# Optimization experiments

Measured on AMD Instinct MI355X. Metric: run time of the kernel, lower is better.

The kernel has to match this reference:

```python
import jax, jax.numpy as jnp
import numpy as np

THRESHOLD = 0.1
EPS = 1e-05


def setup_inputs() -> dict:
    key = jax.random.key(0)
    kx, kl, k1, k2 = jax.random.split(key, 4)
    B, S, D = 8, 4096, 1024
    Dh = max(2, D // 2)
    x = jax.random.normal(kx, (B, S, D), dtype=jnp.float32)
    # trailing (right) padding with random valid lengths in [S//2, S]
    lengths = jax.random.randint(kl, (B,), S // 2, S + 1)
    pad = jnp.arange(S)[None, :] >= lengths[:, None]  # [B, S] bool, True = padded
    W1 = jax.random.normal(k1, (D, Dh), dtype=jnp.float32) * (1.0 / np.sqrt(D))
    b1 = jnp.zeros((Dh,), dtype=jnp.float32)
    W2 = jax.random.normal(k2, (Dh, 1), dtype=jnp.float32) * (1.0 / np.sqrt(Dh))
    b2 = jnp.zeros((1,), dtype=jnp.float32)
    return {"x": x, "pad": pad, "W1": W1, "b1": b1, "W2": W2, "b2": b2}


def reference(x, pad, W1, b1, W2, b2):
    B, S, D = x.shape
    pos = jnp.arange(S)
    # number of valid (non-pad) tokens per batch; pad is trailing
    length = S - jnp.sum(pad, axis=1)  # [B]

    # tiny gate MLP: Linear -> ReLU -> Linear, squashed to (0, 1)
    h = jax.nn.relu(jnp.einsum('bsd,dh->bsh', x, W1) + b1)
    y = jnp.einsum('bsh,ho->bso', h, W2) + b2          # [B, S, 1]
    y = (1.0 + jnp.tanh(10.0 * y)) * 0.5

    # zero out gate values at padded positions (torch loop: y[i, n:] = 0)
    valid = pos[None, :] < length[:, None]             # [B, S]
    y = jnp.where(valid[..., None], y, 0.0)

    # lift so at least one token passes the threshold
    adjust = jnp.clip(EPS + THRESHOLD - jnp.max(y, axis=1), 0.0)  # [B, 1]
    y = y + adjust[:, None, :]                         # broadcast over seq

    u = x * y                                          # gated features [B, S, D]
    ys = y[..., 0]                                     # [B, S]
    u_mask = (ys > THRESHOLD) & (~pad)                 # tokens kept
    new_len = jnp.sum(u_mask, axis=1)                  # [B]

    # compact kept tokens to the front of each row (stable sort: kept first,
    # original order preserved) -- the mask-scatter v[v_mask] = u[u_mask]
    order = jnp.argsort(~u_mask, axis=1, stable=True)  # [B, S]
    v = jnp.take_along_axis(u, order[..., None], axis=1)
    v_mask = pos[None, :] < new_len[:, None]           # [B, S]
    v = jnp.where(v_mask[..., None], v, 0.0)
    v_pad = ~v_mask
    return v, v_pad
```

## Files before the change

kernel.cpp:

```cpp
#include <hip/hip_runtime.h>
#include <math.h>

#define NB 8
#define NS 4096
#define ND 1024
#define NDH 512
#define NTOK (NB*NS)
#define THRESH 0.1f
#define EPSV 1e-5f

using short8   = __attribute__((ext_vector_type(8)))  short;
using floatx16 = __attribute__((ext_vector_type(16))) float;

__device__ __forceinline__ unsigned short f32_to_bf16_rne(float f) {
  union { float f; unsigned u; } v; v.f = f;
  unsigned r = v.u + 0x7fffu + ((v.u >> 16) & 1u);
  return (unsigned short)(r >> 16);
}
__device__ __forceinline__ float bf16_to_f32(unsigned short h) {
  union { unsigned u; float f; } v; v.u = ((unsigned)h) << 16;
  return v.f;
}

__global__ __launch_bounds__(256)
void k0_prep(const float* __restrict__ W1, unsigned short* __restrict__ Wf,
             unsigned int* __restrict__ rowmax) {
  __shared__ float sw[16][513];
  const int t = threadIdx.x;
  const int k16 = blockIdx.x;
  if (k16 == 0 && t < NB) rowmax[t] = 0u;
#pragma unroll
  for (int i = 0; i < 8; ++i) {
    int flat = i * 256 + t;
    int r = flat >> 7, c4 = (flat & 127) << 2;
    *(float4*)&sw[r][c4] = *(const float4*)(W1 + (size_t)(k16 * 16 + r) * NDH + c4);
  }
  __syncthreads();
#pragma unroll
  for (int q = 0; q < 4; ++q) {
    int ss = q * 256 + t;
    int n32 = ss >> 6, lane = ss & 63;
    int n = n32 * 32 + (lane & 31);
    int kb = (lane >> 5) * 8;
    unsigned hi2[4], lo2[4];
#pragma unroll
    for (int j = 0; j < 4; ++j) {
      float w0 = sw[kb + 2 * j][n], w1 = sw[kb + 2 * j + 1][n];
      unsigned short h0 = f32_to_bf16_rne(w0), h1 = f32_to_bf16_rne(w1);
      unsigned short l0 = f32_to_bf16_rne(w0 - bf16_to_f32(h0));
      unsigned short l1 = f32_to_bf16_rne(w1 - bf16_to_f32(h1));
      hi2[j] = (unsigned)h0 | ((unsigned)h1 << 16);
      lo2[j] = (unsigned)l0 | ((unsigned)l1 << 16);
    }
    size_t cb = ((size_t)(n32 * 64 + k16) * 2) * 512 + (size_t)lane * 8;
    *(uint4*)(Wf + cb)       = make_uint4(hi2[0], hi2[1], hi2[2], hi2[3]);
    *(uint4*)(Wf + cb + 512) = make_uint4(lo2[0], lo2[1], lo2[2], lo2[3]);
  }
}

__global__ __launch_bounds__(256, 2)
void k1_gemm(const float* __restrict__ x, const unsigned short* __restrict__ Wf,
             const float* __restrict__ b1, const float* __restrict__ W2,
             float* __restrict__ ylin) {
  __shared__ __align__(16) unsigned short sx[2][2][64 * 40];
  __shared__ float red[4][64];

  const int tid = threadIdx.x;
  const int wave = tid >> 6, lane = tid & 63;
  const int l31 = lane & 31, h5 = lane >> 5;
  const int tok0 = blockIdx.x * 64;

  floatx16 acc[2][4];
#pragma unroll
  for (int mt = 0; mt < 2; ++mt)
#pragma unroll
    for (int nt = 0; nt < 4; ++nt)
#pragma unroll
      for (int r = 0; r < 16; ++r) acc[mt][nt][r] = 0.f;

  const int sm = tid >> 2;
  const int sk = (tid & 3) * 8;
  const float* xrow = x + (size_t)(tok0 + sm) * ND + sk;

  const unsigned short* wb[4];
#pragma unroll
  for (int nt = 0; nt < 4; ++nt)
    wb[nt] = Wf + (((size_t)(wave * 4 + nt) * 64) * 2) * 512 + (size_t)lane * 8;

  for (int it = 0; it < 32; ++it) {
    const int p = it & 1;
    short8 bh[4][2], bl[4][2];
#pragma unroll
    for (int nt = 0; nt < 4; ++nt)
#pragma unroll
      for (int kh = 0; kh < 2; ++kh) {
        const unsigned short* q = wb[nt] + ((size_t)(2 * it + kh) * 2) * 512;
        bh[nt][kh] = *(const short8*)(q);
        bl[nt][kh] = *(const short8*)(q + 512);
      }
    {
      const float* xp = xrow + it * 32;
      float4 xa = *(const float4*)xp;
      float4 xb = *(const float4*)(xp + 4);
      float v8[8] = {xa.x, xa.y, xa.z, xa.w, xb.x, xb.y, xb.z, xb.w};
      unsigned hp[4], lp[4];
#pragma unroll
      for (int j = 0; j < 4; ++j) {
        unsigned short h0 = f32_to_bf16_rne(v8[2 * j]);
        unsigned short h1 = f32_to_bf16_rne(v8[2 * j + 1]);
        unsigned short l0 = f32_to_bf16_rne(v8[2 * j] - bf16_to_f32(h0));
        unsigned short l1 = f32_to_bf16_rne(v8[2 * j + 1] - bf16_to_f32(h1));
        hp[j] = (unsigned)h0 | ((unsigned)h1 << 16);
        lp[j] = (unsigned)l0 | ((unsigned)l1 << 16);
      }
      *(uint4*)&sx[p][0][sm * 40 + sk] = make_uint4(hp[0], hp[1], hp[2], hp[3]);
      *(uint4*)&sx[p][1][sm * 40 + sk] = make_uint4(lp[0], lp[1], lp[2], lp[3]);
    }
    __syncthreads();
    short8 ah[2][2], al[2][2];
#pragma unroll
    for (int mt = 0; mt < 2; ++mt)
#pragma unroll
      for (int kh = 0; kh < 2; ++kh) {
        ah[mt][kh] = *(const short8*)&sx[p][0][(mt * 32 + l31) * 40 + kh * 16 + h5 * 8];
        al[mt][kh] = *(const short8*)&sx[p][1][(mt * 32 + l31) * 40 + kh * 16 + h5 * 8];
      }
#pragma unroll
    for (int kh = 0; kh < 2; ++kh)
#pragma unroll
      for (int nt = 0; nt < 4; ++nt)
#pragma unroll
        for (int mt = 0; mt < 2; ++mt) {
          acc[mt][nt] = __builtin_amdgcn_mfma_f32_32x32x16_bf16(ah[mt][kh], bh[nt][kh], acc[mt][nt], 0, 0, 0);
          acc[mt][nt] = __builtin_amdgcn_mfma_f32_32x32x16_bf16(al[mt][kh], bh[nt][kh], acc[mt][nt], 0, 0, 0);
          acc[mt][nt] = __builtin_amdgcn_mfma_f32_32x32x16_bf16(ah[mt][kh], bl[nt][kh], acc[mt][nt], 0, 0, 0);
        }
  }

  float b1v[4], w2v[4];
#pragma unroll
  for (int nt = 0; nt < 4; ++nt) {
    const int n = wave * 128 + nt * 32 + l31;
    b1v[nt] = b1[n];
    w2v[nt] = W2[n];
  }
#pragma unroll
  for (int mt = 0; mt < 2; ++mt) {
    float pr[16];
#pragma unroll
    for (int r = 0; r < 16; ++r) pr[r] = 0.f;
#pragma unroll
    for (int nt = 0; nt < 4; ++nt)
#pragma unroll
      for (int r = 0; r < 16; ++r)
        pr[r] += fmaxf(acc[mt][nt][r] + b1v[nt], 0.f) * w2v[nt];
#pragma unroll
    for (int m = 1; m <= 16; m <<= 1)
#pragma unroll
      for (int r = 0; r < 16; ++r) pr[r] += __shfl_xor(pr[r], m, 64);
    if (l31 == 0) {
#pragma unroll
      for (int r = 0; r < 16; ++r) {
        int row = (r & 3) + 8 * (r >> 2) + 4 * h5;
        red[wave][mt * 32 + row] = pr[r];
      }
    }
  }
  __syncthreads();
  if (tid < 64)
    ylin[tok0 + tid] = red[0][tid] + red[1][tid] + red[2][tid] + red[3][tid];
}

__global__ __launch_bounds__(256)
void k2a(const float* __restrict__ ylin, const int* __restrict__ pad,
         const float* __restrict__ b2, float* __restrict__ ysq,
         unsigned int* __restrict__ rowmax) {
  __shared__ float wm[4];
  const int t = blockIdx.x * 256 + threadIdx.x;
  float yl = ylin[t] + b2[0];
  float y = (1.f + tanhf(10.f * yl)) * 0.5f;
  if (pad[t]) y = 0.f;
  ysq[t] = y;
  float m = y;
#pragma unroll
  for (int s = 32; s >= 1; s >>= 1) m = fmaxf(m, __shfl_xor(m, s, 64));
  if ((threadIdx.x & 63) == 0) wm[threadIdx.x >> 6] = m;
  __syncthreads();
  if (threadIdx.x == 0) {
    float bm = fmaxf(fmaxf(wm[0], wm[1]), fmaxf(wm[2], wm[3]));
    atomicMax(rowmax + (t >> 12), __float_as_uint(bm));
  }
}

__global__ __launch_bounds__(256)
void k2b(const float* __restrict__ ysq, const int* __restrict__ pad,
         const unsigned int* __restrict__ rowmax, float* __restrict__ yfin,
         int* __restrict__ src_of_dest, int* __restrict__ new_len,
         float* __restrict__ vpad_out) {
  __shared__ int scnt[256];
  const int b = blockIdx.x, tid = threadIdx.x;
  const int base = b * NS, s0 = tid * 16;
  const float adj = fmaxf(EPSV + THRESH - __uint_as_float(rowmax[b]), 0.f);

  float yv[16];
  unsigned km = 0;
  int cnt = 0;
#pragma unroll
  for (int i = 0; i < 16; ++i) {
    int s = s0 + i;
    float yf = ysq[base + s] + adj;
    yv[i] = yf;
    bool keep = (yf > THRESH) && !pad[base + s];
    if (keep) { km |= (1u << i); ++cnt; }
  }
  scnt[tid] = cnt;
  __syncthreads();
  for (int o = 1; o < 256; o <<= 1) {
    int add = (tid >= o) ? scnt[tid - o] : 0;
    __syncthreads();
    scnt[tid] += add;
    __syncthreads();
  }
  const int total = scnt[255];
  int off = scnt[tid] - cnt;
#pragma unroll
  for (int i = 0; i < 16; ++i) {
    int s = s0 + i;
    yfin[base + s] = yv[i];
    if ((km >> i) & 1u) { src_of_dest[base + off] = s; ++off; }
    vpad_out[base + s] = (s >= total) ? 1.f : 0.f;
  }
  if (tid == 0) new_len[b] = total;
}

__global__ __launch_bounds__(256)
void k3_gather(const float* __restrict__ x, const float* __restrict__ yfin,
               const int* __restrict__ src_of_dest, const int* __restrict__ new_len,
               float* __restrict__ v) {
  const int slot0 = blockIdx.x * 4;
  const int b = slot0 >> 12;
  const int nl = new_len[b];
  const int tid = threadIdx.x;
#pragma unroll
  for (int i = 0; i < 4; ++i) {
    const int slot = slot0 + i;
    const int dest = slot & (NS - 1);
    float4* vo = (float4*)(v + (size_t)slot * ND);
    if (dest < nl) {
      const int src = src_of_dest[slot];
      const float g = yfin[b * NS + src];
      const float4* xi = (const float4*)(x + ((size_t)b * NS + src) * ND);
      float4 xv = xi[tid];
      vo[tid] = make_float4(xv.x * g, xv.y * g, xv.z * g, xv.w * g);
    } else {
      vo[tid] = make_float4(0.f, 0.f, 0.f, 0.f);
    }
  }
}

extern "C" void kernel_launch(void* const* d_in, const int* in_sizes, int n_in,
                              void* d_out, int out_size, void* d_ws, size_t ws_size,
                              hipStream_t stream) {
  const float* x   = (const float*)d_in[0];
  const int*   pad = (const int*)d_in[1];
  const float* W1  = (const float*)d_in[2];
  const float* b1  = (const float*)d_in[3];
  const float* W2  = (const float*)d_in[4];
  const float* b2  = (const float*)d_in[5];

  float* v    = (float*)d_out;
  float* vpad = v + (size_t)NTOK * ND;

  unsigned short* Wf = (unsigned short*)(v + 24000000);
  float* ysq = v + 26000000;

  float* ylin = (float*)d_ws;
  float* yfin = ylin + NTOK;
  int* src    = (int*)(yfin + NTOK);
  int* nlen   = src + NTOK;
  unsigned int* rowmax = (unsigned int*)(nlen + NB);

  k0_prep<<<64, 256, 0, stream>>>(W1, Wf, rowmax);
  k1_gemm<<<NTOK / 64, 256, 0, stream>>>(x, Wf, b1, W2, ylin);
  k2a<<<NTOK / 256, 256, 0, stream>>>(ylin, pad, b2, ysq, rowmax);
  k2b<<<NB, 256, 0, stream>>>(ysq, pad, rowmax, yfin, src, nlen, vpad);
  k3_gather<<<NTOK / 4, 256, 0, stream>>>(x, yfin, src, nlen, v);
}
```

Before: 321.9 us.

## Prefetch next x tile in GEMM, fuse gate epilogue, streamline scan and gather

The GEMM loop now prefetches the next K-slice of x into registers and converts it into the other shared buffer while MFMAs run, leaving a single barrier per iteration. The separate tanh/mask/rowmax kernel is folded into the GEMM epilogue, which drops one launch and the ylin round trip. The prefix scan in k2b uses wave shuffles instead of a barrier-heavy shared-memory scan and writes gate values compacted by destination. The gather processes 16 slots per block with nontemporal stores. Risks are more register pressure in the GEMM and more atomics on rowmax, one per 64-token block.

Result: no change. 323.5 us (+0.5%).

```diff
diff --git a/kernel.cpp b/kernel.cpp
--- a/kernel.cpp
+++ b/kernel.cpp
@@ -11,6 +11,7 @@
 
 using short8   = __attribute__((ext_vector_type(8)))  short;
 using floatx16 = __attribute__((ext_vector_type(16))) float;
+using floatv4  = __attribute__((ext_vector_type(4)))  float;
 
 __device__ __forceinline__ unsigned short f32_to_bf16_rne(float f) {
   union { float f; unsigned u; } v; v.f = f;
@@ -61,7 +62,8 @@
 __global__ __launch_bounds__(256, 2)
 void k1_gemm(const float* __restrict__ x, const unsigned short* __restrict__ Wf,
              const float* __restrict__ b1, const float* __restrict__ W2,
-             float* __restrict__ ylin) {
+             const int* __restrict__ pad, const float* __restrict__ b2,
+             float* __restrict__ ysq, unsigned int* __restrict__ rowmax) {
   __shared__ __align__(16) unsigned short sx[2][2][64 * 40];
   __shared__ float red[4][64];
 
@@ -87,8 +89,27 @@
   for (int nt = 0; nt < 4; ++nt)
     wb[nt] = Wf + (((size_t)(wave * 4 + nt) * 64) * 2) * 512 + (size_t)lane * 8;
 
+  {
+    float4 xa = *(const float4*)xrow;
+    float4 xb = *(const float4*)(xrow + 4);
+    float v8[8] = {xa.x, xa.y, xa.z, xa.w, xb.x, xb.y, xb.z, xb.w};
+    unsigned hp[4], lp[4];
+#pragma unroll
+    for (int j = 0; j < 4; ++j) {
+      unsigned short h0 = f32_to_bf16_rne(v8[2 * j]);
+      unsigned short h1 = f32_to_bf16_rne(v8[2 * j + 1]);
+      unsigned short l0 = f32_to_bf16_rne(v8[2 * j] - bf16_to_f32(h0));
+      unsigned short l1 = f32_to_bf16_rne(v8[2 * j + 1] - bf16_to_f32(h1));
+      hp[j] = (unsigned)h0 | ((unsigned)h1 << 16);
+      lp[j] = (unsigned)l0 | ((unsigned)l1 << 16);
+    }
+    *(uint4*)&sx[0][0][sm * 40 + sk] = make_uint4(hp[0], hp[1], hp[2], hp[3]);
+    *(uint4*)&sx[0][1][sm * 40 + sk] = make_uint4(lp[0], lp[1], lp[2], lp[3]);
+  }
+
   for (int it = 0; it < 32; ++it) {
     const int p = it & 1;
+    __syncthreads();
     short8 bh[4][2], bl[4][2];
 #pragma unroll
     for (int nt = 0; nt < 4; ++nt)
@@ -98,11 +119,32 @@
         bh[nt][kh] = *(const short8*)(q);
         bl[nt][kh] = *(const short8*)(q + 512);
       }
-    {
-      const float* xp = xrow + it * 32;
-      float4 xa = *(const float4*)xp;
-      float4 xb = *(const float4*)(xp + 4);
-      float v8[8] = {xa.x, xa.y, xa.z, xa.w, xb.x, xb.y, xb.z, xb.w};
+    float4 pxa, pxb;
+    if (it < 31) {
+      const float* xp = xrow + (it + 1) * 32;
+      pxa = *(const float4*)xp;
+      pxb = *(const float4*)(xp + 4);
+    }
+    short8 ah[2][2], al[2][2];
+#pragma unroll
+    for (int mt = 0; mt < 2; ++mt)
+#pragma unroll
+      for (int kh = 0; kh < 2; ++kh) {
+        ah[mt][kh] = *(const short8*)&sx[p][0][(mt * 32 + l31) * 40 + kh * 16 + h5 * 8];
+        al[mt][kh] = *(const short8*)&sx[p][1][(mt * 32 + l31) * 40 + kh * 16 + h5 * 8];
+      }
+#pragma unroll
+    for (int nt = 0; nt < 4; ++nt)
+#pragma unroll
+      for (int kh = 0; kh < 2; ++kh)
+#pragma unroll
+        for (int mt = 0; mt < 2; ++mt) {
+          acc[mt][nt] = __builtin_amdgcn_mfma_f32_32x32x16_bf16(ah[mt][kh], bh[nt][kh], acc[mt][nt], 0, 0, 0);
+          acc[mt][nt] = __builtin_amdgcn_mfma_f32_32x32x16_bf16(al[mt][kh], bh[nt][kh], acc[mt][nt], 0, 0, 0);
+          acc[mt][nt] = __builtin_amdgcn_mfma_f32_32x32x16_bf16(ah[mt][kh], bl[nt][kh], acc[mt][nt], 0, 0, 0);
+        }
+    if (it < 31) {
+      float v8[8] = {pxa.x, pxa.y, pxa.z, pxa.w, pxb.x, pxb.y, pxb.z, pxb.w};
       unsigned hp[4], lp[4];
 #pragma unroll
       for (int j = 0; j < 4; ++j) {
@@ -113,28 +155,9 @@
         hp[j] = (unsigned)h0 | ((unsigned)h1 << 16);
         lp[j] = (unsigned)l0 | ((unsigned)l1 << 16);
       }
-      *(uint4*)&sx[p][0][sm * 40 + sk] = make_uint4(hp[0], hp[1], hp[2], hp[3]);
-      *(uint4*)&sx[p][1][sm * 40 + sk] = make_uint4(lp[0], lp[1], lp[2], lp[3]);
-    }
-    __syncthreads();
-    short8 ah[2][2], al[2][2];
-#pragma unroll
-    for (int mt = 0; mt < 2; ++mt)
-#pragma unroll
-      for (int kh = 0; kh < 2; ++kh) {
-        ah[mt][kh] = *(const short8*)&sx[p][0][(mt * 32 + l31) * 40 + kh * 16 + h5 * 8];
-        al[mt][kh] = *(const short8*)&sx[p][1][(mt * 32 + l31) * 40 + kh * 16 + h5 * 8];
-      }
-#pragma unroll
-    for (int kh = 0; kh < 2; ++kh)
-#pragma unroll
-      for (int nt = 0; nt < 4; ++nt)
-#pragma unroll
-        for (int mt = 0; mt < 2; ++mt) {
-          acc[mt][nt] = __builtin_amdgcn_mfma_f32_32x32x16_bf16(ah[mt][kh], bh[nt][kh], acc[mt][nt], 0, 0, 0);
-          acc[mt][nt] = __builtin_amdgcn_mfma_f32_32x32x16_bf16(al[mt][kh], bh[nt][kh], acc[mt][nt], 0, 0, 0);
-          acc[mt][nt] = __builtin_amdgcn_mfma_f32_32x32x16_bf16(ah[mt][kh], bl[nt][kh], acc[mt][nt], 0, 0, 0);
-        }
+      *(uint4*)&sx[p ^ 1][0][sm * 40 + sk] = make_uint4(hp[0], hp[1], hp[2], hp[3]);
+      *(uint4*)&sx[p ^ 1][1][sm * 40 + sk] = make_uint4(lp[0], lp[1], lp[2], lp[3]);
+    }
   }
 
   float b1v[4], w2v[4];
@@ -167,38 +190,28 @@
     }
   }
   __syncthreads();
-  if (tid < 64)
-    ylin[tok0 + tid] = red[0][tid] + red[1][tid] + red[2][tid] + red[3][tid];
-}
-
-__global__ __launch_bounds__(256)
-void k2a(const float* __restrict__ ylin, const int* __restrict__ pad,
-         const float* __restrict__ b2, float* __restrict__ ysq,
-         unsigned int* __restrict__ rowmax) {
-  __shared__ float wm[4];
-  const int t = blockIdx.x * 256 + threadIdx.x;
-  float yl = ylin[t] + b2[0];
-  float y = (1.f + tanhf(10.f * yl)) * 0.5f;
-  if (pad[t]) y = 0.f;
-  ysq[t] = y;
-  float m = y;
-#pragma unroll
-  for (int s = 32; s >= 1; s >>= 1) m = fmaxf(m, __shfl_xor(m, s, 64));
-  if ((threadIdx.x & 63) == 0) wm[threadIdx.x >> 6] = m;
-  __syncthreads();
-  if (threadIdx.x == 0) {
-    float bm = fmaxf(fmaxf(wm[0], wm[1]), fmaxf(wm[2], wm[3]));
-    atomicMax(rowmax + (t >> 12), __float_as_uint(bm));
+  if (tid < 64) {
+    float s = red[0][tid] + red[1][tid] + red[2][tid] + red[3][tid];
+    const int t = tok0 + tid;
+    float yl = s + b2[0];
+    float y = (1.f + tanhf(10.f * yl)) * 0.5f;
+    if (pad[t]) y = 0.f;
+    ysq[t] = y;
+    float m = y;
+#pragma unroll
+    for (int o = 32; o >= 1; o >>= 1) m = fmaxf(m, __shfl_xor(m, o, 64));
+    if (tid == 0) atomicMax(rowmax + (t >> 12), __float_as_uint(m));
   }
 }
 
 __global__ __launch_bounds__(256)
 void k2b(const float* __restrict__ ysq, const int* __restrict__ pad,
-         const unsigned int* __restrict__ rowmax, float* __restrict__ yfin,
+         const unsigned int* __restrict__ rowmax, float* __restrict__ gval,
          int* __restrict__ src_of_dest, int* __restrict__ new_len,
          float* __restrict__ vpad_out) {
-  __shared__ int scnt[256];
+  __shared__ int ssum[4];
   const int b = blockIdx.x, tid = threadIdx.x;
+  const int lane = tid & 63, wv = tid >> 6;
   const int base = b * NS, s0 = tid * 16;
   const float adj = fmaxf(EPSV + THRESH - __uint_as_float(rowmax[b]), 0.f);
 
@@ -213,48 +226,54 @@
     bool keep = (yf > THRESH) && !pad[base + s];
     if (keep) { km |= (1u << i); ++cnt; }
   }
-  scnt[tid] = cnt;
+  int inc = cnt;
+#pragma unroll
+  for (int o = 1; o < 64; o <<= 1) {
+    int tmp = __shfl_up(inc, o, 64);
+    if (lane >= o) inc += tmp;
+  }
+  if (lane == 63) ssum[wv] = inc;
   __syncthreads();
-  for (int o = 1; o < 256; o <<= 1) {
-    int add = (tid >= o) ? scnt[tid - o] : 0;
-    __syncthreads();
-    scnt[tid] += add;
-    __syncthreads();
-  }
-  const int total = scnt[255];
-  int off = scnt[tid] - cnt;
+  int wpre = 0;
+  for (int w = 0; w < wv; ++w) wpre += ssum[w];
+  const int total = ssum[0] + ssum[1] + ssum[2] + ssum[3];
+  int off = wpre + inc - cnt;
 #pragma unroll
   for (int i = 0; i < 16; ++i) {
     int s = s0 + i;
-    yfin[base + s] = yv[i];
-    if ((km >> i) & 1u) { src_of_dest[base + off] = s; ++off; }
+    if ((km >> i) & 1u) {
+      src_of_dest[base + off] = s;
+      gval[base + off] = yv[i];
+      ++off;
+    }
     vpad_out[base + s] = (s >= total) ? 1.f : 0.f;
   }
   if (tid == 0) new_len[b] = total;
 }
 
 __global__ __launch_bounds__(256)
-void k3_gather(const float* __restrict__ x, const float* __restrict__ yfin,
+void k3_gather(const float* __restrict__ x, const float* __restrict__ gval,
                const int* __restrict__ src_of_dest, const int* __restrict__ new_len,
                float* __restrict__ v) {
-  const int slot0 = blockIdx.x * 4;
+  const int slot0 = blockIdx.x * 16;
   const int b = slot0 >> 12;
   const int nl = new_len[b];
   const int tid = threadIdx.x;
 #pragma unroll
-  for (int i = 0; i < 4; ++i) {
+  for (int i = 0; i < 16; ++i) {
     const int slot = slot0 + i;
     const int dest = slot & (NS - 1);
-    float4* vo = (float4*)(v + (size_t)slot * ND);
+    floatv4* vo = (floatv4*)(v + (size_t)slot * ND);
+    floatv4 r;
     if (dest < nl) {
       const int src = src_of_dest[slot];
-      const float g = yfin[b * NS + src];
-      const float4* xi = (const float4*)(x + ((size_t)b * NS + src) * ND);
-      float4 xv = xi[tid];
-      vo[tid] = make_float4(xv.x * g, xv.y * g, xv.z * g, xv.w * g);
+      const float g = gval[slot];
+      floatv4 xv = ((const floatv4*)(x + ((size_t)b * NS + src) * ND))[tid];
+      r = xv * g;
     } else {
-      vo[tid] = make_float4(0.f, 0.f, 0.f, 0.f);
-    }
+      r = (floatv4)(0.f);
+    }
+    __builtin_nontemporal_store(r, vo + tid);
   }
 }
 
@@ -272,17 +291,15 @@
   float* vpad = v + (size_t)NTOK * ND;
 
   unsigned short* Wf = (unsigned short*)(v + 24000000);
-  float* ysq = v + 26000000;
-
-  float* ylin = (float*)d_ws;
-  float* yfin = ylin + NTOK;
-  int* src    = (int*)(yfin + NTOK);
+
+  float* ysq  = (float*)d_ws;
+  float* gval = ysq + NTOK;
+  int* src    = (int*)(gval + NTOK);
   int* nlen   = src + NTOK;
   unsigned int* rowmax = (unsigned int*)(nlen + NB);
 
   k0_prep<<<64, 256, 0, stream>>>(W1, Wf, rowmax);
-  k1_gemm<<<NTOK / 64, 256, 0, stream>>>(x, Wf, b1, W2, ylin);
-  k2a<<<NTOK / 256, 256, 0, stream>>>(ylin, pad, b2, ysq, rowmax);
-  k2b<<<NB, 256, 0, stream>>>(ysq, pad, rowmax, yfin, src, nlen, vpad);
-  k3_gather<<<NTOK / 4, 256, 0, stream>>>(x, yfin, src, nlen, v);
-}
+  k1_gemm<<<NTOK / 64, 256, 0, stream>>>(x, Wf, b1, W2, pad, b2, ysq, rowmax);
+  k2b<<<NB, 256, 0, stream>>>(ysq, pad, rowmax, gval, src, nlen, vpad);
+  k3_gather<<<NTOK / 16, 256, 0, stream>>>(x, gval, src, nlen, v);
+}
```
